# Performance work log

Hardware: AMD Instinct MI355X
Metric: run time of the kernel (lower is better)

## Reference

```python
import jax, jax.numpy as jnp
import numpy as np

B, T, F, H = 128, 512, 128, 512
ODE_STEPS = 2
MAX_DT = 1.0


def setup_inputs() -> dict:
    key = jax.random.key(0)
    ks = jax.random.split(key, 8)
    xavier = lambda k, shape: jax.random.uniform(
        k, shape, jnp.float32, -1.0, 1.0) * np.sqrt(6.0 / (shape[0] + shape[1]))
    return {
        "x": jax.random.normal(ks[0], (B, T, F), jnp.float32),
        "time_diffs": jax.random.uniform(ks[1], (B, T), jnp.float32),
        "Wz": xavier(ks[2], (H, F + H)), "bz": jnp.zeros((H,), jnp.float32),
        "Wr": xavier(ks[3], (H, F + H)), "br": jnp.zeros((H,), jnp.float32),
        "Wg": xavier(ks[4], (H, F + H)), "bg": jnp.zeros((H,), jnp.float32),
    }


def reference(x, time_diffs, Wz, bz, Wr, br, Wg, bg):
    hidden = Wz.shape[0]

    def ode_func(x_t, h):
        # dh/dt = (1 - z) * (g - h)
        xh = jnp.concatenate([x_t, h], axis=-1)           # [b, F+H]
        z = jax.nn.sigmoid(xh @ Wz.T + bz)
        r = jax.nn.sigmoid(xh @ Wr.T + br)
        g = jnp.tanh(jnp.concatenate([x_t, r * h], axis=-1) @ Wg.T + bg)
        return (1.0 - z) * (g - h)

    def rk4(x_t, h, dt):
        k1 = ode_func(x_t, h)
        k2 = ode_func(x_t, h + 0.5 * dt * k1)
        k3 = ode_func(x_t, h + 0.5 * dt * k2)
        k4 = ode_func(x_t, h + dt * k3)
        return h + (dt / 6.0) * (k1 + 2.0 * k2 + 2.0 * k3 + k4)

    def step(h, inp):
        x_t, td = inp                                     # [b,F], [b]
        dt = (jnp.minimum(td, MAX_DT) / ODE_STEPS)[:, None]
        for _ in range(ODE_STEPS):                        # small fixed count
            h = rk4(x_t, h, dt)
        return h, h

    h0 = jnp.zeros((x.shape[0], hidden), x.dtype)
    _, out = jax.lax.scan(step, h0, (jnp.swapaxes(x, 0, 1), time_diffs.T))
    return jnp.swapaxes(out, 0, 1)                        # [b, T, H]
```

## Files before the change

### kernel.cpp

```cpp
#include <hip/hip_runtime.h>


namespace {
constexpr int kB = 128, kT = 512, kF = 128, kH = 512, kFH = 640;
constexpr int QZ4 = 0, QR4 = 16384, QG4 = 32768;
constexpr int WXZ4 = 49152, WXR4 = 57344, WXG4 = 65536;
constexpr size_t CS_OFF = (size_t)73728 * 16;
constexpr size_t AXP_OFF = 1310720;
constexpr size_t AXP_BYTES = (size_t)kB * kT * 3 * kH * 2;
constexpr float HSCL = 100.0f;
}

typedef _Float16 h2_t __attribute__((ext_vector_type(2)));

__device__ __forceinline__ unsigned short f2h(float f) {
  return __builtin_bit_cast(unsigned short, (_Float16)f);
}
__device__ __forceinline__ unsigned pack2h(float a, float b) {
  return (unsigned)f2h(a) | ((unsigned)f2h(b) << 16);
}
__device__ __forceinline__ float h2f(unsigned short u) {
  return (float)__builtin_bit_cast(_Float16, u);
}
__device__ __forceinline__ float dot2(unsigned w, unsigned h, float acc) {
  return __builtin_amdgcn_fdot2(__builtin_bit_cast(h2_t, w),
                                __builtin_bit_cast(h2_t, h), acc, false);
}
__device__ __forceinline__ float dot2x4(uint4 w, uint4 h, float acc) {
  acc = dot2(w.x, h.x, acc); acc = dot2(w.y, h.y, acc);
  acc = dot2(w.z, h.z, acc); acc = dot2(w.w, h.w, acc);
  return acc;
}
__device__ __forceinline__ uint4 pk8(const float* s) {
  const float4 a = *(const float4*)s;
  const float4 b = *(const float4*)(s + 4);
  uint4 o;
  o.x = pack2h(a.x, a.y); o.y = pack2h(a.z, a.w);
  o.z = pack2h(b.x, b.y); o.w = pack2h(b.z, b.w);
  return o;
}
__device__ __forceinline__ int sd4(unsigned a, unsigned b, int acc) {
  return __builtin_amdgcn_sdot4((int)a, (int)b, acc, false);
}
__device__ __forceinline__ void dslice(const uint4 w, const unsigned* hq,
                                       int p, int& acc) {
  acc = sd4(w.x, hq[4 * p + 0], acc);
  acc = sd4(w.y, hq[4 * p + 1], acc);
  acc = sd4(w.z, hq[4 * p + 2], acc);
  acc = sd4(w.w, hq[4 * p + 3], acc);
}

#define DECL_OPQ(v, ptr, s)                                          \
  uint4 v = (ptr)[(s) * kH];                                         \
  asm volatile("" : "+v"(v.x), "+v"(v.y), "+v"(v.z), "+v"(v.w))

__global__ void quant_weights(const float* __restrict__ Wz,
                              const float* __restrict__ Wr,
                              const float* __restrict__ Wg,
                              void* __restrict__ ws) {
  const int bx = blockIdx.x;
  const int gate = bx >> 9, j = bx & 511;
  const float* W = (gate == 0) ? Wz : (gate == 1) ? Wr : Wg;
  const float* row = W + (size_t)j * kFH;
  const int lane = threadIdx.x;
  uint4* ws4 = (uint4*)ws;

  const float* src = row + kF + lane * 8;
  float v[8]; float m = 0.f;
#pragma unroll
  for (int i = 0; i < 8; ++i) { v[i] = src[i]; m = fmaxf(m, fabsf(v[i])); }
#pragma unroll
  for (int off = 32; off; off >>= 1) m = fmaxf(m, __shfl_xor(m, off));
  const float inv = 127.f / m;
  unsigned u0 = 0, u1 = 0;
#pragma unroll
  for (int i = 0; i < 4; ++i) {
    int q = __float2int_rn(v[i] * inv); q = max(-127, min(127, q));
    u0 |= ((unsigned)(q & 255)) << (8 * i);
  }
#pragma unroll
  for (int i = 0; i < 4; ++i) {
    int q = __float2int_rn(v[4 + i] * inv); q = max(-127, min(127, q));
    u1 |= ((unsigned)(q & 255)) << (8 * i);
  }
  const int p = lane >> 1, sub = lane & 1;
  const int qbase = (gate == 0) ? QZ4 : (gate == 1) ? QR4 : QG4;
  *(uint2*)((char*)ws + ((size_t)(qbase + p * kH + j)) * 16 + sub * 8) =
      make_uint2(u0, u1);
  if (lane < 16) {
    const int xbase = (gate == 0) ? WXZ4 : (gate == 1) ? WXR4 : WXG4;
    ws4[xbase + lane * kH + j] = pk8(row + lane * 8);
  }
  if (lane == 0)
    ((float*)((char*)ws + CS_OFF))[gate * 512 + j] = m / (127.f * HSCL);
}

__global__ __launch_bounds__(512) void xpart_pre(
    const float* __restrict__ x, const float* __restrict__ bz,
    const float* __restrict__ br, const float* __restrict__ bg,
    const uint4* __restrict__ ws, unsigned short* __restrict__ axp) {
  __shared__ unsigned xt[8][64];
  const int bx = blockIdx.x;
  const int b = bx >> 6;
  const int t0 = (bx & 63) * 8;
  const int tid = threadIdx.x;
  {
    const int m = tid >> 6, c = tid & 63;
    const float2 xv =
        *(const float2*)(x + ((size_t)b * kT + t0 + m) * kF + 2 * c);
    xt[m][c] = pack2h(xv.x, xv.y);
  }
  __syncthreads();
#pragma unroll
  for (int gate = 0; gate < 3; ++gate) {
    const uint4* wx =
        ws + ((gate == 0) ? WXZ4 : (gate == 1) ? WXR4 : WXG4) + tid;
    const float bv = ((gate == 0) ? bz : (gate == 1) ? br : bg)[tid];
    float acc[8];
#pragma unroll
    for (int m = 0; m < 8; ++m) acc[m] = bv;
#pragma unroll
    for (int p = 0; p < 16; ++p) {
      const uint4 w = wx[p * kH];
#pragma unroll
      for (int m = 0; m < 8; ++m)
        acc[m] = dot2x4(w, ((const uint4*)xt[m])[p], acc[m]);
    }
#pragma unroll
    for (int m = 0; m < 8; ++m)
      axp[(((size_t)b * kT + t0 + m) * 3 + gate) * kH + tid] = f2h(acc[m]);
  }
}

template <int XPRE>
__global__ __launch_bounds__(1024, 4) void cgru_i8s(
    const float* __restrict__ x, const float* __restrict__ td,
    const float* __restrict__ bz, const float* __restrict__ br,
    const float* __restrict__ bg, const uint4* __restrict__ ws,
    const unsigned short* __restrict__ axp, float* __restrict__ out) {
  __shared__ uint4 WLa[2][6][kH];
  __shared__ uint4 WLg[2][3][kH];
  __shared__ unsigned hq[kH / 4];
  __shared__ unsigned rq[kH / 4];
  __shared__ unsigned xpk[kF / 2];
  __shared__ float gpart[kH];

  const int b = blockIdx.x;
  const int tid = threadIdx.x;
  const int j = tid & (kH - 1);
  const int half = tid >> 9;

  const uint4* __restrict__ wQa = ws + (half ? QR4 : QZ4) + j;
  const uint4* __restrict__ wQg = ws + QG4 + j;
  const uint4* __restrict__ wxa = ws + (half ? WXR4 : WXZ4) + j;
  const uint4* __restrict__ wxg = ws + WXG4 + j;
  const float* cs = (const float*)((const char*)ws + CS_OFF);
  const float csa = cs[(half ? 512 : 0) + j];
  const float csg = cs[1024 + j];

  DECL_OPQ(a0, wQa, 0); DECL_OPQ(a1, wQa, 1); DECL_OPQ(a2, wQa, 2);
  DECL_OPQ(a3, wQa, 3); DECL_OPQ(a4, wQa, 4); DECL_OPQ(a5, wQa, 5);
  DECL_OPQ(a6, wQa, 6); DECL_OPQ(a7, wQa, 7);
  {
    const uint4* qa = ws + (half ? QR4 : QZ4);
#pragma unroll
    for (int q = 0; q < 6; ++q) WLa[half][q][j] = qa[(8 + q) * kH + j];
#pragma unroll
    for (int q = 0; q < 3; ++q)
      WLg[half][q][j] = (ws + QG4)[((half ? 16 : 0) + q) * kH + j];
  }

  const float ba = half ? br[j] : bz[j];
  const float bgv = bg[j];
  float hb = 0.f, hs = 0.f, kacc = 0.f, zv = 0.f, dtv = 0.f;
  if (tid < kH / 4) hq[tid] = 0;
  if constexpr (XPRE) __syncthreads();

  for (int t = 0; t < kT; ++t) {
    float ax, agx;
    if constexpr (XPRE) {
      const size_t bt3 = ((size_t)b * kT + t) * 3;
      ax = h2f(axp[(bt3 + half) * kH + j]);
      agx = half ? 0.f : h2f(axp[(bt3 + 2) * kH + j]);
      if (half == 0) dtv = fminf(td[(size_t)b * kT + t], 1.0f) * 0.5f;
    } else {
      if (tid < kF / 2) {
        const float2 xv =
            *(const float2*)(x + ((size_t)b * kT + t) * kF + 2 * tid);
        xpk[tid] = pack2h(xv.x, xv.y);
      }
      __syncthreads();
      const uint4* xp4 = (const uint4*)xpk;
      ax = ba;
#pragma unroll 4
      for (int p = 0; p < 16; ++p) ax = dot2x4(wxa[p * kH], xp4[p], ax);
      agx = half ? 0.f : bgv;
#pragma unroll 4
      for (int p = 0; p < 8; ++p)
        agx = dot2x4(wxg[(half * 8 + p) * kH], xp4[half * 8 + p], agx);
      if (half == 0) dtv = fminf(td[(size_t)b * kT + t], 1.0f) * 0.5f;
    }

    for (int e = 0; e < 8; ++e) {
      const int s = e & 3;
      int ah = 0;
      dslice(a0, hq, 0, ah); dslice(a1, hq, 1, ah);
      dslice(a2, hq, 2, ah); dslice(a3, hq, 3, ah);
      dslice(a4, hq, 4, ah); dslice(a5, hq, 5, ah);
      dslice(a6, hq, 6, ah); dslice(a7, hq, 7, ah);
#pragma unroll
      for (int q = 0; q < 6; ++q)
        dslice(WLa[half][q][j], hq, 8 + q, ah);
#pragma unroll 6
      for (int p = 14; p < 32; ++p)
        dslice(wQa[p * kH], hq, p, ah);
      const float aA = ax + csa * (float)ah;

      if (half == 0) {
        zv = 1.0f / (1.0f + __expf(-aA));
      } else {
        const float r = 1.0f / (1.0f + __expf(-aA));
        const float hv = (float)((const char*)hq)[j] * (1.0f / HSCL);
        int q = __float2int_rn(fminf(fmaxf(r * hv, -1.27f), 1.27f) * HSCL);
        ((char*)rq)[j] = (char)q;
      }
      __syncthreads();

      int gh = 0;
      const int bs = half << 4;
#pragma unroll
      for (int q = 0; q < 3; ++q)
        dslice(WLg[half][q][j], rq, bs + q, gh);
#pragma unroll 4
      for (int p = bs + 3; p < bs + 16; ++p)
        dslice(wQg[p * kH], rq, p, gh);
      const float gp = agx + csg * (float)gh;
      if (half == 1) gpart[j] = gp;
      __syncthreads();

      if (half == 0) {
        const float g = tanhf(gp + gpart[j]);
        const float kk = (1.0f - zv) * (g - hs);
        kacc = (s == 0) ? kk : kacc + ((s == 3) ? 1.0f : 2.0f) * kk;
        float nxt;
        if (s < 3) {
          nxt = fmaf((s == 2 ? 1.0f : 0.5f) * dtv, kk, hb);
        } else {
          hb = fmaf(dtv * (1.0f / 6.0f), kacc, hb);
          nxt = hb;
        }
        hs = nxt;
        int q = __float2int_rn(fminf(fmaxf(nxt, -1.27f), 1.27f) * HSCL);
        ((char*)hq)[j] = (char)q;
      }
      __syncthreads();
    }

    if (half == 0) out[((size_t)b * kT + t) * kH + j] = hb;
  }
}

extern "C" void kernel_launch(void* const* d_in, const int* in_sizes, int n_in,
                              void* d_out, int out_size, void* d_ws, size_t ws_size,
                              hipStream_t stream) {
  const float* x  = (const float*)d_in[0];
  const float* td = (const float*)d_in[1];
  const float* Wz = (const float*)d_in[2];
  const float* bz = (const float*)d_in[3];
  const float* Wr = (const float*)d_in[4];
  const float* br = (const float*)d_in[5];
  const float* Wg = (const float*)d_in[6];
  const float* bg = (const float*)d_in[7];
  float* out = (float*)d_out;

  quant_weights<<<3 * kH, 64, 0, stream>>>(Wz, Wr, Wg, d_ws);

  unsigned short* axp = (unsigned short*)((char*)d_ws + AXP_OFF);
  if (ws_size >= AXP_OFF + AXP_BYTES) {
    xpart_pre<<<kB * (kT / 8), 512, 0, stream>>>(
        x, bz, br, bg, (const uint4*)d_ws, axp);
    cgru_i8s<1><<<kB, 1024, 0, stream>>>(
        x, td, bz, br, bg, (const uint4*)d_ws, axp, out);
  } else {
    cgru_i8s<0><<<kB, 1024, 0, stream>>>(
        x, td, bz, br, bg, (const uint4*)d_ws, axp, out);
  }
}
```

Baseline: 19.36 ms.

## Split hidden-dim reduction across wave halves with shuffle combine, drop one barrier

Reorganizes the per-batch recurrent kernel. Each hidden unit is now handled by two lanes that split the K dimension in half: one lane per half computes the z, r and g dot products over its K half, and the partials are combined with a cross-lane shuffle instead of assigning the z and r gates to separate thread halves. This removes the gpart shared-memory exchange and one __syncthreads per RK stage, and every thread now computes the gating math redundantly. The register-resident and LDS-resident weight slices are re-split per K half for both z and r, which changes register pressure and LDS layout.

```diff
diff --git a/kernel.cpp b/kernel.cpp
--- a/kernel.cpp
+++ b/kernel.cpp
@@ -133,56 +133,56 @@
 }
 
 template <int XPRE>
-__global__ __launch_bounds__(1024, 4) void cgru_i8s(
+__global__ __launch_bounds__(1024, 4) void cgru_i8p(
     const float* __restrict__ x, const float* __restrict__ td,
     const float* __restrict__ bz, const float* __restrict__ br,
     const float* __restrict__ bg, const uint4* __restrict__ ws,
     const unsigned short* __restrict__ axp, float* __restrict__ out) {
-  __shared__ uint4 WLa[2][6][kH];
+  __shared__ uint4 WLz[2][3][kH];
+  __shared__ uint4 WLr[2][3][kH];
   __shared__ uint4 WLg[2][3][kH];
   __shared__ unsigned hq[kH / 4];
   __shared__ unsigned rq[kH / 4];
   __shared__ unsigned xpk[kF / 2];
-  __shared__ float gpart[kH];
 
   const int b = blockIdx.x;
   const int tid = threadIdx.x;
-  const int j = tid & (kH - 1);
-  const int half = tid >> 9;
-
-  const uint4* __restrict__ wQa = ws + (half ? QR4 : QZ4) + j;
-  const uint4* __restrict__ wQg = ws + QG4 + j;
-  const uint4* __restrict__ wxa = ws + (half ? WXR4 : WXZ4) + j;
+  const int kh = (tid >> 5) & 1;
+  const int j = ((tid >> 6) << 5) | (tid & 31);
+  const int sb = kh << 4;
+
+  const uint4* __restrict__ wz = ws + QZ4 + j;
+  const uint4* __restrict__ wr = ws + QR4 + j;
+  const uint4* __restrict__ wg = ws + QG4 + j;
+  const uint4* __restrict__ wxz = ws + WXZ4 + j;
+  const uint4* __restrict__ wxr = ws + WXR4 + j;
   const uint4* __restrict__ wxg = ws + WXG4 + j;
   const float* cs = (const float*)((const char*)ws + CS_OFF);
-  const float csa = cs[(half ? 512 : 0) + j];
-  const float csg = cs[1024 + j];
-
-  DECL_OPQ(a0, wQa, 0); DECL_OPQ(a1, wQa, 1); DECL_OPQ(a2, wQa, 2);
-  DECL_OPQ(a3, wQa, 3); DECL_OPQ(a4, wQa, 4); DECL_OPQ(a5, wQa, 5);
-  DECL_OPQ(a6, wQa, 6); DECL_OPQ(a7, wQa, 7);
-  {
-    const uint4* qa = ws + (half ? QR4 : QZ4);
-#pragma unroll
-    for (int q = 0; q < 6; ++q) WLa[half][q][j] = qa[(8 + q) * kH + j];
-#pragma unroll
-    for (int q = 0; q < 3; ++q)
-      WLg[half][q][j] = (ws + QG4)[((half ? 16 : 0) + q) * kH + j];
-  }
-
-  const float ba = half ? br[j] : bz[j];
-  const float bgv = bg[j];
-  float hb = 0.f, hs = 0.f, kacc = 0.f, zv = 0.f, dtv = 0.f;
+  const float csz = cs[j], csr = cs[512 + j], csg = cs[1024 + j];
+
+  DECL_OPQ(z0, wz, sb + 0); DECL_OPQ(z1, wz, sb + 1);
+  DECL_OPQ(z2, wz, sb + 2); DECL_OPQ(z3, wz, sb + 3);
+  DECL_OPQ(r0, wr, sb + 0); DECL_OPQ(r1, wr, sb + 1);
+  DECL_OPQ(r2, wr, sb + 2); DECL_OPQ(r3, wr, sb + 3);
+#pragma unroll
+  for (int q = 0; q < 3; ++q) {
+    WLz[kh][q][j] = wz[(sb + 4 + q) * kH];
+    WLr[kh][q][j] = wr[(sb + 4 + q) * kH];
+    WLg[kh][q][j] = wg[(sb + q) * kH];
+  }
+
+  const float bzv = bz[j], brv = br[j], bgv = bg[j];
+  float hb = 0.f, hs = 0.f, kacc = 0.f;
   if (tid < kH / 4) hq[tid] = 0;
-  if constexpr (XPRE) __syncthreads();
+  __syncthreads();
 
   for (int t = 0; t < kT; ++t) {
-    float ax, agx;
+    float axz, axr, axg;
     if constexpr (XPRE) {
       const size_t bt3 = ((size_t)b * kT + t) * 3;
-      ax = h2f(axp[(bt3 + half) * kH + j]);
-      agx = half ? 0.f : h2f(axp[(bt3 + 2) * kH + j]);
-      if (half == 0) dtv = fminf(td[(size_t)b * kT + t], 1.0f) * 0.5f;
+      axz = h2f(axp[(bt3 + 0) * kH + j]);
+      axr = h2f(axp[(bt3 + 1) * kH + j]);
+      axg = h2f(axp[(bt3 + 2) * kH + j]);
     } else {
       if (tid < kF / 2) {
         const float2 xv =
@@ -191,72 +191,76 @@
       }
       __syncthreads();
       const uint4* xp4 = (const uint4*)xpk;
-      ax = ba;
+      axz = bzv; axr = brv; axg = bgv;
 #pragma unroll 4
-      for (int p = 0; p < 16; ++p) ax = dot2x4(wxa[p * kH], xp4[p], ax);
-      agx = half ? 0.f : bgv;
-#pragma unroll 4
-      for (int p = 0; p < 8; ++p)
-        agx = dot2x4(wxg[(half * 8 + p) * kH], xp4[half * 8 + p], agx);
-      if (half == 0) dtv = fminf(td[(size_t)b * kT + t], 1.0f) * 0.5f;
+      for (int p = 0; p < 16; ++p) {
+        const uint4 xv = xp4[p];
+        axz = dot2x4(wxz[p * kH], xv, axz);
+        axr = dot2x4(wxr[p * kH], xv, axr);
+        axg = dot2x4(wxg[p * kH], xv, axg);
+      }
+      __syncthreads();
     }
+    const float dtv = fminf(td[(size_t)b * kT + t], 1.0f) * 0.5f;
 
     for (int e = 0; e < 8; ++e) {
       const int s = e & 3;
-      int ah = 0;
-      dslice(a0, hq, 0, ah); dslice(a1, hq, 1, ah);
-      dslice(a2, hq, 2, ah); dslice(a3, hq, 3, ah);
-      dslice(a4, hq, 4, ah); dslice(a5, hq, 5, ah);
-      dslice(a6, hq, 6, ah); dslice(a7, hq, 7, ah);
-#pragma unroll
-      for (int q = 0; q < 6; ++q)
-        dslice(WLa[half][q][j], hq, 8 + q, ah);
-#pragma unroll 6
-      for (int p = 14; p < 32; ++p)
-        dslice(wQa[p * kH], hq, p, ah);
-      const float aA = ax + csa * (float)ah;
-
-      if (half == 0) {
-        zv = 1.0f / (1.0f + __expf(-aA));
+      int za = 0, ra = 0;
+      dslice(z0, hq, sb + 0, za); dslice(r0, hq, sb + 0, ra);
+      dslice(z1, hq, sb + 1, za); dslice(r1, hq, sb + 1, ra);
+      dslice(z2, hq, sb + 2, za); dslice(r2, hq, sb + 2, ra);
+      dslice(z3, hq, sb + 3, za); dslice(r3, hq, sb + 3, ra);
+#pragma unroll
+      for (int q = 0; q < 3; ++q) {
+        dslice(WLz[kh][q][j], hq, sb + 4 + q, za);
+        dslice(WLr[kh][q][j], hq, sb + 4 + q, ra);
+      }
+#pragma unroll 3
+      for (int p = sb + 7; p < sb + 16; ++p) {
+        dslice(wz[p * kH], hq, p, za);
+        dslice(wr[p * kH], hq, p, ra);
+      }
+      za += __shfl_xor(za, 32);
+      ra += __shfl_xor(ra, 32);
+      const float aZ = axz + csz * (float)za;
+      const float aR = axr + csr * (float)ra;
+      const float zv = 1.0f / (1.0f + __expf(-aZ));
+      const float rv = 1.0f / (1.0f + __expf(-aR));
+      const float rh = rv * hs;
+      if (kh == 0) {
+        int q = __float2int_rn(fminf(fmaxf(rh, -1.27f), 1.27f) * HSCL);
+        ((char*)rq)[j] = (char)q;
+      }
+      __syncthreads();
+
+      int ga = 0;
+#pragma unroll
+      for (int q = 0; q < 3; ++q)
+        dslice(WLg[kh][q][j], rq, sb + q, ga);
+#pragma unroll 4
+      for (int p = sb + 3; p < sb + 16; ++p)
+        dslice(wg[p * kH], rq, p, ga);
+      ga += __shfl_xor(ga, 32);
+      const float g = tanhf(axg + csg * (float)ga);
+
+      const float kk = (1.0f - zv) * (g - hs);
+      kacc = (s == 0) ? kk : kacc + ((s == 3) ? 1.0f : 2.0f) * kk;
+      float nxt;
+      if (s < 3) {
+        nxt = fmaf((s == 2 ? 1.0f : 0.5f) * dtv, kk, hb);
       } else {
-        const float r = 1.0f / (1.0f + __expf(-aA));
-        const float hv = (float)((const char*)hq)[j] * (1.0f / HSCL);
-        int q = __float2int_rn(fminf(fmaxf(r * hv, -1.27f), 1.27f) * HSCL);
-        ((char*)rq)[j] = (char)q;
-      }
-      __syncthreads();
-
-      int gh = 0;
-      const int bs = half << 4;
-#pragma unroll
-      for (int q = 0; q < 3; ++q)
-        dslice(WLg[half][q][j], rq, bs + q, gh);
-#pragma unroll 4
-      for (int p = bs + 3; p < bs + 16; ++p)
-        dslice(wQg[p * kH], rq, p, gh);
-      const float gp = agx + csg * (float)gh;
-      if (half == 1) gpart[j] = gp;
-      __syncthreads();
-
-      if (half == 0) {
-        const float g = tanhf(gp + gpart[j]);
-        const float kk = (1.0f - zv) * (g - hs);
-        kacc = (s == 0) ? kk : kacc + ((s == 3) ? 1.0f : 2.0f) * kk;
-        float nxt;
-        if (s < 3) {
-          nxt = fmaf((s == 2 ? 1.0f : 0.5f) * dtv, kk, hb);
-        } else {
-          hb = fmaf(dtv * (1.0f / 6.0f), kacc, hb);
-          nxt = hb;
-        }
-        hs = nxt;
+        hb = fmaf(dtv * (1.0f / 6.0f), kacc, hb);
+        nxt = hb;
+      }
+      hs = nxt;
+      if (kh == 0) {
         int q = __float2int_rn(fminf(fmaxf(nxt, -1.27f), 1.27f) * HSCL);
         ((char*)hq)[j] = (char)q;
       }
       __syncthreads();
     }
 
-    if (half == 0) out[((size_t)b * kT + t) * kH + j] = hb;
+    if (kh == 0) out[((size_t)b * kT + t) * kH + j] = hb;
   }
 }
 
@@ -279,10 +283,10 @@
   if (ws_size >= AXP_OFF + AXP_BYTES) {
     xpart_pre<<<kB * (kT / 8), 512, 0, stream>>>(
         x, bz, br, bg, (const uint4*)d_ws, axp);
-    cgru_i8s<1><<<kB, 1024, 0, stream>>>(
+    cgru_i8p<1><<<kB, 1024, 0, stream>>>(
         x, td, bz, br, bg, (const uint4*)d_ws, axp, out);
   } else {
-    cgru_i8s<0><<<kB, 1024, 0, stream>>>(
+    cgru_i8p<0><<<kB, 1024, 0, stream>>>(
         x, td, bz, br, bg, (const uint4*)d_ws, axp, out);
   }
 }
```

After: 19.44 ms. About the same (+0.4%).
